# Kernel tuning notes

Hardware: AMD Instinct MI355X
Metric: run time of the kernel (lower is better)

Reference implementation:

```python
import jax, jax.numpy as jnp
import numpy as np

B, E, F, H, C = 2048, 16, 512, 1024, 512
TOP_K = 4
TEMP = 1.0


def setup_inputs() -> dict:
    key = jax.random.key(0)
    ks = jax.random.split(key, 5)
    h = jax.random.normal(ks[0], (B, F), jnp.float32)
    # Router posterior params (xavier-ish mu, logvar init at -7 as in torch code)
    W_mu = jax.random.normal(ks[1], (E, F), jnp.float32) * (1.0 / np.sqrt(F))
    W_logvar = jnp.full((E, F), -7.0, jnp.float32)
    b_mu = jnp.zeros((E,), jnp.float32)
    b_logvar = jnp.full((E,), -7.0, jnp.float32)
    # Expert MLP params: layer1 [F->H] relu, layer2 [H->C]
    W1 = jax.random.normal(ks[2], (E, F, H), jnp.float32) * (1.0 / np.sqrt(F))
    b1 = jnp.zeros((E, H), jnp.float32)
    W2 = jax.random.normal(ks[3], (E, H, C), jnp.float32) * (1.0 / np.sqrt(H))
    b2 = jnp.zeros((E, C), jnp.float32)
    return {"h": h, "W_mu": W_mu, "b_mu": b_mu, "W_logvar": W_logvar,
            "b_logvar": b_logvar, "W1": W1, "b1": b1, "W2": W2, "b2": b2}


def reference(h, W_mu, b_mu, W_logvar, b_logvar, W1, b1, W2, b2):
    # Bayesian router moments: mu = h @ W_mu^T + b_mu ; var = (h*h) @ exp(W_logvar)^T + exp(b_logvar)
    mu_m = h @ W_mu.T + b_mu                                   # [B,E]
    var_m = (h * h) @ jnp.exp(W_logvar).T + jnp.exp(b_logvar)  # [B,E]
    var_m = jnp.maximum(var_m, 1e-12)
    # Logistic-normal shrink: tilde = mu / sqrt(1 + (pi/8) var)
    tilde_m = mu_m / jnp.sqrt(1.0 + (jnp.pi / 8.0) * var_m)
    gate_probs = jax.nn.softmax(tilde_m / TEMP, axis=-1)       # [B,E]
    # Strict top-k by gate_scores (tilde_m), renormalize probs within top-k
    topk_scores, topk_idx = jax.lax.top_k(tilde_m, TOP_K)      # [B,k]
    topk_w = jnp.take_along_axis(gate_probs, topk_idx, axis=1) # [B,k]
    topk_w = topk_w / jnp.maximum(topk_w.sum(axis=1, keepdims=True), 1e-12)
    # Dense combine weights: w[b,e] = sum of renormalized top-k weights of token b for expert e
    Bsz = h.shape[0]
    w = jnp.zeros((Bsz, E), h.dtype).at[jnp.arange(Bsz)[:, None], topk_idx].add(topk_w)
    # Expert MLPs (grouped GEMM form); tokens not routed to expert e get weight 0
    a = jax.nn.relu(jnp.einsum('bf,efh->beh', h, W1) + b1)     # [B,E,H]
    y = jnp.einsum('beh,ehc->bec', a, W2) + b2                 # [B,E,C]
    combined = jnp.einsum('be,bec->bc', w, y)                  # [B,C]
    return combined
```

## Files before the change

kernel.cpp:

```cpp
#include <hip/hip_runtime.h>
#include <hip/hip_bf16.h>

typedef __attribute__((ext_vector_type(8))) short bf16x8;
typedef __attribute__((ext_vector_type(4))) float f32x4;

#define NTOK   2048
#define NEXP   16
#define NF     512
#define NH     1024
#define NCOUT  512
#define NPAIR  8192

__device__ __forceinline__ void gload16_lds(const __hip_bfloat16* g, const __hip_bfloat16* l) {
  __builtin_amdgcn_global_load_lds((const __attribute__((address_space(1))) void*)g,
                                   (__attribute__((address_space(3))) void*)l, 16, 0, 0);
}

__global__ __launch_bounds__(256) void precompute_kernel(
    const float* __restrict__ W_logvar, const float* __restrict__ b_logvar,
    float* __restrict__ expW, float* __restrict__ expb)
{
  int i = blockIdx.x * 256 + threadIdx.x;
  if (i < NEXP * NF) expW[i] = expf(W_logvar[i]);
  if (i < NEXP) expb[i] = expf(b_logvar[i]);
}

__global__ __launch_bounds__(256) void router_kernel(
    const float* __restrict__ h, const float* __restrict__ W_mu,
    const float* __restrict__ b_mu, const float* __restrict__ expW,
    const float* __restrict__ expb,
    int* __restrict__ topk_idx, float* __restrict__ topk_w,
    __hip_bfloat16* __restrict__ hb)
{
  __shared__ __align__(16) float hs[NF], hs2[NF];
  __shared__ float smu[NEXP], svar[NEXP];
  const int b = blockIdx.x, tid = threadIdx.x;
  for (int i = tid; i < NF; i += 256) {
    float v = h[(size_t)b * NF + i];
    hs[i] = v; hs2[i] = v * v;
    hb[(size_t)b * NF + i] = __float2bfloat16(v);
  }
  __syncthreads();
  const int e = tid >> 4, l = tid & 15;
  float mu = 0.f, var = 0.f;
  const float4* wm4 = (const float4*)(W_mu + e * NF);
  const float4* wv4 = (const float4*)(expW + e * NF);
  const float4* h4  = (const float4*)hs;
  const float4* h24 = (const float4*)hs2;
#pragma unroll
  for (int j = 0; j < NF / 64; ++j) {
    int i4 = l + j * 16;
    float4 a = h4[i4],  wa = wm4[i4];
    float4 c = h24[i4], wc = wv4[i4];
    mu  += a.x * wa.x + a.y * wa.y + a.z * wa.z + a.w * wa.w;
    var += c.x * wc.x + c.y * wc.y + c.z * wc.z + c.w * wc.w;
  }
#pragma unroll
  for (int o = 1; o < 16; o <<= 1) { mu += __shfl_xor(mu, o); var += __shfl_xor(var, o); }
  if (l == 0) { smu[e] = mu + b_mu[e]; svar[e] = var + expb[e]; }
  __syncthreads();
  if (tid < 64) {
    float val = -1e30f;
    if (tid < NEXP) {
      float v = fmaxf(svar[tid], 1e-12f);
      val = smu[tid] / sqrtf(1.0f + 0.39269908169872414f * v);
    }
    float mx = 0.f, wsum = 0.f;
    int i0, i1, i2, i3; float p0, p1, p2, p3;
#define TOPK_ROUND(ii, pp, FIRST)                                          \
    {                                                                      \
      float m = val;                                                       \
      m = fmaxf(m, __shfl_xor(m, 1));  m = fmaxf(m, __shfl_xor(m, 2));     \
      m = fmaxf(m, __shfl_xor(m, 4));  m = fmaxf(m, __shfl_xor(m, 8));     \
      m = fmaxf(m, __shfl_xor(m, 16)); m = fmaxf(m, __shfl_xor(m, 32));    \
      unsigned long long bm = __ballot(val == m);                          \
      int bi = (int)__builtin_ctzll(bm);                                   \
      if (FIRST) mx = m;                                                   \
      pp = expf(m - mx); wsum += pp; ii = bi;                              \
      if (tid == bi) val = -1e30f;                                         \
    }
    TOPK_ROUND(i0, p0, 1)
    TOPK_ROUND(i1, p1, 0)
    TOPK_ROUND(i2, p2, 0)
    TOPK_ROUND(i3, p3, 0)
#undef TOPK_ROUND
    if (tid == 0) {
      float inv = 1.0f / fmaxf(wsum, 1e-12f);
      topk_idx[b * 4 + 0] = i0; topk_w[b * 4 + 0] = p0 * inv;
      topk_idx[b * 4 + 1] = i1; topk_w[b * 4 + 1] = p1 * inv;
      topk_idx[b * 4 + 2] = i2; topk_w[b * 4 + 2] = p2 * inv;
      topk_idx[b * 4 + 3] = i3; topk_w[b * 4 + 3] = p3 * inv;
    }
  }
}

__global__ __launch_bounds__(1024) void route_finish_kernel(
    const int* __restrict__ topk_idx,
    int* __restrict__ counts, int* __restrict__ offsets,
    int* __restrict__ token_of_row, int* __restrict__ pair_row)
{
  __shared__ int cnt[128][16];
  __shared__ int choff[128][16];
  __shared__ int tot[16];
  __shared__ int soff[16];
  const int tid = threadIdx.x;
  const int wv = tid >> 6, ln = tid & 63;
  int mye[8], myrank[8];
#pragma unroll
  for (int r = 0; r < 8; ++r) {
    const int chunk = r * 16 + wv;
    const int t = chunk * 64 + ln;
    const int e = topk_idx[t];
    mye[r] = e;
    unsigned long long mymask = 0;
#pragma unroll
    for (int ee = 0; ee < 16; ++ee) {
      unsigned long long b = __ballot(e == ee);
      if (ln == 0) cnt[chunk][ee] = __popcll(b);
      if (e == ee) mymask = b;
    }
    myrank[r] = __popcll(mymask & ((1ull << ln) - 1ull));
  }
  __syncthreads();
  if (tid < 16) {
    int run = 0;
    for (int c = 0; c < 128; ++c) { choff[c][tid] = run; run += cnt[c][tid]; }
    tot[tid] = run;
    counts[tid] = run;
  }
  __syncthreads();
  if (tid == 0) {
    int run = 0;
    for (int e2 = 0; e2 < NEXP; ++e2) { soff[e2] = run; offsets[e2] = run; run += tot[e2]; }
  }
  __syncthreads();
#pragma unroll
  for (int r = 0; r < 8; ++r) {
    const int chunk = r * 16 + wv;
    const int t = chunk * 64 + ln;
    const int e = mye[r];
    const int pos = soff[e] + choff[chunk][e] + myrank[r];
    token_of_row[pos] = t >> 2;
    pair_row[t] = pos;
  }
}

__global__ __launch_bounds__(256) void transpose_convert_kernel(
    const float* __restrict__ in, __hip_bfloat16* __restrict__ out, int R, int C)
{
  __shared__ float tile[64][33];
  const int e = blockIdx.z;
  const int r0 = blockIdx.y * 64, c0 = blockIdx.x * 32;
  const int x = threadIdx.x & 31, y = threadIdx.x >> 5;
  const float* ip = in + ((size_t)e * R + r0) * C + c0;
#pragma unroll
  for (int i = 0; i < 8; ++i) tile[y + 8 * i][x] = ip[(size_t)(y + 8 * i) * C + x];
  __syncthreads();
  const int rp = threadIdx.x & 31, cb = threadIdx.x >> 5;
#pragma unroll
  for (int j = 0; j < 4; ++j) {
    const int c = cb + 8 * j;
    union { __hip_bfloat16 b[2]; unsigned u; } v;
    v.b[0] = __float2bfloat16(tile[2 * rp][c]);
    v.b[1] = __float2bfloat16(tile[2 * rp + 1][c]);
    *(unsigned*)(out + ((size_t)e * C + c0 + c) * R + r0 + 2 * rp) = v.u;
  }
}


__global__ __launch_bounds__(256) void gemm1_kernel(
    const __hip_bfloat16* __restrict__ hb,
    const __hip_bfloat16* __restrict__ W1t,
    const float* __restrict__ b1,
    const int* __restrict__ token_of_row, const int* __restrict__ offsets,
    const int* __restrict__ counts,
    __hip_bfloat16* __restrict__ a_out)
{
  const int bid = blockIdx.x;
  const int id  = (bid & 7) * 512 + (bid >> 3);
  const int e   = id >> 8;
  const int m0  = ((id >> 4) & 15) * 128;
  const int n0  = (id & 15) * 64;
  const int cnt = counts[e];
  if (m0 >= cnt) return;
  const int off = offsets[e];

  __shared__ __align__(16) __hip_bfloat16 As[2][128 * 64];
  __shared__ __align__(16) __hip_bfloat16 Bs[2][64 * 64];

  const int tid = threadIdx.x;
  const int w = tid >> 6, l = tid & 63;
  const int wm = w >> 1, wn = w & 1;
  const int r16 = l & 15, g4 = l >> 4;
  const int sx = r16 & 7;
  const int koffL = (((l & 7) ^ (l >> 3)) * 8);

  const __hip_bfloat16* Aptr[4];
#pragma unroll
  for (int i = 0; i < 4; ++i) {
    int r = off + m0 + w * 32 + i * 8 + (l >> 3);
    if (r > NPAIR - 1) r = NPAIR - 1;
    Aptr[i] = hb + (size_t)token_of_row[r] * NF + koffL;
  }
  const __hip_bfloat16* Bptr[2];
#pragma unroll
  for (int i = 0; i < 2; ++i)
    Bptr[i] = W1t + ((size_t)e * NH + n0 + w * 16 + i * 8 + (l >> 3)) * NF + koffL;

#define STG1(b, k0) { \
  _Pragma("unroll") for (int i = 0; i < 4; ++i) gload16_lds(Aptr[i] + (k0), &As[b][(w * 32 + i * 8) * 64]); \
  _Pragma("unroll") for (int i = 0; i < 2; ++i) gload16_lds(Bptr[i] + (k0), &Bs[b][(w * 16 + i * 8) * 64]); }

  f32x4 acc[4][2] = {};
  const int NT = NF / 64;

  STG1(0, 0)
  for (int t = 0; t < NT; ++t) {
    __syncthreads();
    const int cur = t & 1;
    if (t + 1 < NT) STG1(cur ^ 1, (t + 1) * 64)
#pragma unroll
    for (int ks = 0; ks < 2; ++ks) {
      const int seg = (ks * 4 + g4) ^ sx;
      bf16x8 af[4], bq[2];
#pragma unroll
      for (int rr = 0; rr < 4; ++rr)
        af[rr] = *(const bf16x8*)(&As[cur][(wm * 64 + rr * 16 + r16) * 64 + seg * 8]);
#pragma unroll
      for (int nn = 0; nn < 2; ++nn)
        bq[nn] = *(const bf16x8*)(&Bs[cur][(wn * 32 + nn * 16 + r16) * 64 + seg * 8]);
#pragma unroll
      for (int rr = 0; rr < 4; ++rr)
#pragma unroll
        for (int nn = 0; nn < 2; ++nn)
          acc[rr][nn] = __builtin_amdgcn_mfma_f32_16x16x32_bf16(af[rr], bq[nn], acc[rr][nn], 0, 0, 0);
    }
  }
#undef STG1

  const int q4 = l >> 4, cl = l & 15;
  const int mmax = cnt - m0;
#pragma unroll
  for (int rr = 0; rr < 4; ++rr) {
#pragma unroll
    for (int nn = 0; nn < 2; ++nn) {
      const int c = n0 + wn * 32 + nn * 16 + cl;
      const float bias = b1[e * NH + c];
#pragma unroll
      for (int q = 0; q < 4; ++q) {
        const int r = wm * 64 + rr * 16 + q4 * 4 + q;
        if (r < mmax) {
          float v = fmaxf(acc[rr][nn][q] + bias, 0.f);
          a_out[(size_t)(off + m0 + r) * NH + c] = __float2bfloat16(v);
        }
      }
    }
  }
}

__global__ __launch_bounds__(256) void gemm2_kernel(
    const __hip_bfloat16* __restrict__ a_in,
    const __hip_bfloat16* __restrict__ W2t,
    const float* __restrict__ b2,
    const int* __restrict__ offsets, const int* __restrict__ counts,
    float* __restrict__ ybuf)
{
  const int bid = blockIdx.x;
  const int id  = (bid & 7) * 256 + (bid >> 3);
  const int e   = id >> 7;
  const int m0  = ((id >> 3) & 15) * 128;
  const int n0  = (id & 7) * 64;
  const int cnt = counts[e];
  if (m0 >= cnt) return;
  const int off = offsets[e];

  __shared__ __align__(16) __hip_bfloat16 As[2][128 * 64];
  __shared__ __align__(16) __hip_bfloat16 Bs[2][64 * 64];

  const int tid = threadIdx.x;
  const int w = tid >> 6, l = tid & 63;
  const int wm = w >> 1, wn = w & 1;
  const int r16 = l & 15, g4 = l >> 4;
  const int sx = r16 & 7;
  const int koffL = (((l & 7) ^ (l >> 3)) * 8);

  const __hip_bfloat16* Aptr[4];
#pragma unroll
  for (int i = 0; i < 4; ++i) {
    int r = off + m0 + w * 32 + i * 8 + (l >> 3);
    if (r > NPAIR - 1) r = NPAIR - 1;
    Aptr[i] = a_in + (size_t)r * NH + koffL;
  }
  const __hip_bfloat16* Bptr[2];
#pragma unroll
  for (int i = 0; i < 2; ++i)
    Bptr[i] = W2t + ((size_t)e * NCOUT + n0 + w * 16 + i * 8 + (l >> 3)) * NH + koffL;

#define STG2(b, k0) { \
  _Pragma("unroll") for (int i = 0; i < 4; ++i) gload16_lds(Aptr[i] + (k0), &As[b][(w * 32 + i * 8) * 64]); \
  _Pragma("unroll") for (int i = 0; i < 2; ++i) gload16_lds(Bptr[i] + (k0), &Bs[b][(w * 16 + i * 8) * 64]); }

  f32x4 acc[4][2] = {};
  const int NT = NH / 64;

  STG2(0, 0)
  for (int t = 0; t < NT; ++t) {
    __syncthreads();
    const int cur = t & 1;
    if (t + 1 < NT) STG2(cur ^ 1, (t + 1) * 64)
#pragma unroll
    for (int ks = 0; ks < 2; ++ks) {
      const int seg = (ks * 4 + g4) ^ sx;
      bf16x8 af[4], bq[2];
#pragma unroll
      for (int rr = 0; rr < 4; ++rr)
        af[rr] = *(const bf16x8*)(&As[cur][(wm * 64 + rr * 16 + r16) * 64 + seg * 8]);
#pragma unroll
      for (int nn = 0; nn < 2; ++nn)
        bq[nn] = *(const bf16x8*)(&Bs[cur][(wn * 32 + nn * 16 + r16) * 64 + seg * 8]);
#pragma unroll
      for (int rr = 0; rr < 4; ++rr)
#pragma unroll
        for (int nn = 0; nn < 2; ++nn)
          acc[rr][nn] = __builtin_amdgcn_mfma_f32_16x16x32_bf16(af[rr], bq[nn], acc[rr][nn], 0, 0, 0);
    }
  }
#undef STG2

  const int q4 = l >> 4, cl = l & 15;
  const int mmax = cnt - m0;
#pragma unroll
  for (int rr = 0; rr < 4; ++rr) {
#pragma unroll
    for (int nn = 0; nn < 2; ++nn) {
      const int c = n0 + wn * 32 + nn * 16 + cl;
      const float bias = b2[e * NCOUT + c];
#pragma unroll
      for (int q = 0; q < 4; ++q) {
        const int r = wm * 64 + rr * 16 + q4 * 4 + q;
        if (r < mmax)
          ybuf[(size_t)(off + m0 + r) * NCOUT + c] = acc[rr][nn][q] + bias;
      }
    }
  }
}

__global__ __launch_bounds__(256) void combine_kernel(
    const float* __restrict__ ybuf, const int* __restrict__ pair_row,
    const float* __restrict__ topk_w, float* __restrict__ out)
{
  const int tok = blockIdx.x;
  const int c = threadIdx.x * 2;
  float a0 = 0.f, a1 = 0.f;
#pragma unroll
  for (int k = 0; k < 4; ++k) {
    const int t = tok * 4 + k;
    const float wt = topk_w[t];
    const float2 y = *(const float2*)(ybuf + (size_t)pair_row[t] * NCOUT + c);
    a0 += wt * y.x; a1 += wt * y.y;
  }
  *(float2*)(out + (size_t)tok * NCOUT + c) = make_float2(a0, a1);
}

extern "C" void kernel_launch(void* const* d_in, const int* in_sizes, int n_in,
                              void* d_out, int out_size, void* d_ws, size_t ws_size,
                              hipStream_t stream) {
  (void)in_sizes; (void)n_in; (void)ws_size; (void)out_size;
  const float* h        = (const float*)d_in[0];
  const float* W_mu     = (const float*)d_in[1];
  const float* b_mu     = (const float*)d_in[2];
  const float* W_logvar = (const float*)d_in[3];
  const float* b_logvar = (const float*)d_in[4];
  const float* W1       = (const float*)d_in[5];
  const float* b1       = (const float*)d_in[6];
  const float* W2       = (const float*)d_in[7];
  const float* b2       = (const float*)d_in[8];
  float* out = (float*)d_out;

  char* p = (char*)d_ws;
  int*   counts   = (int*)p;   p += 16 * 4;
  int*   offsets  = (int*)p;   p += 16 * 4;
  float* expb     = (float*)p; p += 16 * 4;
  p += 16 * 4;
  float* expW     = (float*)p; p += (size_t)NEXP * NF * 4;
  int*   topk_idx = (int*)p;   p += (size_t)NPAIR * 4;
  float* topk_w   = (float*)p; p += (size_t)NPAIR * 4;
  int*   tok_row  = (int*)p;   p += (size_t)NPAIR * 4;
  int*   pair_row = (int*)p;   p += (size_t)NPAIR * 4;
  __hip_bfloat16* hb   = (__hip_bfloat16*)p; p += (size_t)NTOK * NF * 2;
  __hip_bfloat16* W1t  = (__hip_bfloat16*)p; p += (size_t)NEXP * NF * NH * 2;
  __hip_bfloat16* W2t  = (__hip_bfloat16*)p; p += (size_t)NEXP * NH * NCOUT * 2;
  __hip_bfloat16* abuf = (__hip_bfloat16*)p; p += (size_t)NPAIR * NH * 2;
  float*          ybuf = (float*)p;          p += (size_t)NPAIR * NCOUT * 4;

  precompute_kernel<<<(NEXP * NF + 255) / 256, 256, 0, stream>>>(W_logvar, b_logvar, expW, expb);
  router_kernel<<<NTOK, 256, 0, stream>>>(h, W_mu, b_mu, expW, expb, topk_idx, topk_w, hb);
  route_finish_kernel<<<1, 1024, 0, stream>>>(topk_idx, counts, offsets, tok_row, pair_row);

  transpose_convert_kernel<<<dim3(NH / 32, NF / 64, NEXP), 256, 0, stream>>>(W1, W1t, NF, NH);
  transpose_convert_kernel<<<dim3(NCOUT / 32, NH / 64, NEXP), 256, 0, stream>>>(W2, W2t, NH, NCOUT);

  gemm1_kernel<<<4096, 256, 0, stream>>>(hb, W1t, b1, tok_row, offsets, counts, abuf);
  gemm2_kernel<<<2048, 256, 0, stream>>>(abuf, W2t, b2, offsets, counts, ybuf);
  combine_kernel<<<NTOK, 256, 0, stream>>>(ybuf, pair_row, topk_w, out);
}
```

Baseline: 102.6 us.

## Fuse exp into router, split route_finish across blocks, single-buffer GEMM staging

Drops the separate precompute kernel and computes exp of the logvar weights inside the router, removing one launch at the cost of redundant exp work per token block. route_finish now runs on 8 blocks, each scattering rows for two experts while recomputing the shared counts. Both GEMM kernels switch from double-buffered LDS staging to a single buffer with a sync on each side of the load. This cuts LDS use and may raise occupancy, but load latency is no longer hidden behind MFMA work.

```diff
diff --git a/kernel.cpp b/kernel.cpp
--- a/kernel.cpp
+++ b/kernel.cpp
@@ -16,19 +16,10 @@
                                    (__attribute__((address_space(3))) void*)l, 16, 0, 0);
 }
 
-__global__ __launch_bounds__(256) void precompute_kernel(
-    const float* __restrict__ W_logvar, const float* __restrict__ b_logvar,
-    float* __restrict__ expW, float* __restrict__ expb)
-{
-  int i = blockIdx.x * 256 + threadIdx.x;
-  if (i < NEXP * NF) expW[i] = expf(W_logvar[i]);
-  if (i < NEXP) expb[i] = expf(b_logvar[i]);
-}
-
 __global__ __launch_bounds__(256) void router_kernel(
     const float* __restrict__ h, const float* __restrict__ W_mu,
-    const float* __restrict__ b_mu, const float* __restrict__ expW,
-    const float* __restrict__ expb,
+    const float* __restrict__ b_mu, const float* __restrict__ W_logvar,
+    const float* __restrict__ b_logvar,
     int* __restrict__ topk_idx, float* __restrict__ topk_w,
     __hip_bfloat16* __restrict__ hb)
 {
@@ -44,7 +35,7 @@
   const int e = tid >> 4, l = tid & 15;
   float mu = 0.f, var = 0.f;
   const float4* wm4 = (const float4*)(W_mu + e * NF);
-  const float4* wv4 = (const float4*)(expW + e * NF);
+  const float4* wv4 = (const float4*)(W_logvar + e * NF);
   const float4* h4  = (const float4*)hs;
   const float4* h24 = (const float4*)hs2;
 #pragma unroll
@@ -53,11 +44,11 @@
     float4 a = h4[i4],  wa = wm4[i4];
     float4 c = h24[i4], wc = wv4[i4];
     mu  += a.x * wa.x + a.y * wa.y + a.z * wa.z + a.w * wa.w;
-    var += c.x * wc.x + c.y * wc.y + c.z * wc.z + c.w * wc.w;
+    var += c.x * __expf(wc.x) + c.y * __expf(wc.y) + c.z * __expf(wc.z) + c.w * __expf(wc.w);
   }
 #pragma unroll
   for (int o = 1; o < 16; o <<= 1) { mu += __shfl_xor(mu, o); var += __shfl_xor(var, o); }
-  if (l == 0) { smu[e] = mu + b_mu[e]; svar[e] = var + expb[e]; }
+  if (l == 0) { smu[e] = mu + b_mu[e]; svar[e] = var + __expf(b_logvar[e]); }
   __syncthreads();
   if (tid < 64) {
     float val = -1e30f;
@@ -100,11 +91,12 @@
     int* __restrict__ token_of_row, int* __restrict__ pair_row)
 {
   __shared__ int cnt[128][16];
-  __shared__ int choff[128][16];
+  __shared__ int choff[128][2];
   __shared__ int tot[16];
   __shared__ int soff[16];
   const int tid = threadIdx.x;
   const int wv = tid >> 6, ln = tid & 63;
+  const int e0 = blockIdx.x * 2;
   int mye[8], myrank[8];
 #pragma unroll
   for (int r = 0; r < 8; ++r) {
@@ -115,33 +107,44 @@
     unsigned long long mymask = 0;
 #pragma unroll
     for (int ee = 0; ee < 16; ++ee) {
-      unsigned long long b = __ballot(e == ee);
-      if (ln == 0) cnt[chunk][ee] = __popcll(b);
-      if (e == ee) mymask = b;
+      unsigned long long bmask = __ballot(e == ee);
+      if (ln == 0) cnt[chunk][ee] = __popcll(bmask);
+      if (e == ee) mymask = bmask;
     }
     myrank[r] = __popcll(mymask & ((1ull << ln) - 1ull));
   }
   __syncthreads();
   if (tid < 16) {
     int run = 0;
-    for (int c = 0; c < 128; ++c) { choff[c][tid] = run; run += cnt[c][tid]; }
+    for (int c = 0; c < 128; ++c) run += cnt[c][tid];
     tot[tid] = run;
-    counts[tid] = run;
+    if (blockIdx.x == 0) counts[tid] = run;
+  }
+  if (tid >= 32 && tid < 34) {
+    const int e = e0 + (tid - 32);
+    int run = 0;
+    for (int c = 0; c < 128; ++c) { choff[c][tid - 32] = run; run += cnt[c][e]; }
   }
   __syncthreads();
   if (tid == 0) {
     int run = 0;
-    for (int e2 = 0; e2 < NEXP; ++e2) { soff[e2] = run; offsets[e2] = run; run += tot[e2]; }
+    for (int e2 = 0; e2 < NEXP; ++e2) {
+      soff[e2] = run;
+      if (blockIdx.x == 0) offsets[e2] = run;
+      run += tot[e2];
+    }
   }
   __syncthreads();
 #pragma unroll
   for (int r = 0; r < 8; ++r) {
-    const int chunk = r * 16 + wv;
-    const int t = chunk * 64 + ln;
     const int e = mye[r];
-    const int pos = soff[e] + choff[chunk][e] + myrank[r];
-    token_of_row[pos] = t >> 2;
-    pair_row[t] = pos;
+    if (e == e0 || e == e0 + 1) {
+      const int chunk = r * 16 + wv;
+      const int t = chunk * 64 + ln;
+      const int pos = soff[e] + choff[chunk][e - e0] + myrank[r];
+      token_of_row[pos] = t >> 2;
+      pair_row[t] = pos;
+    }
   }
 }
 
@@ -185,8 +188,8 @@
   if (m0 >= cnt) return;
   const int off = offsets[e];
 
-  __shared__ __align__(16) __hip_bfloat16 As[2][128 * 64];
-  __shared__ __align__(16) __hip_bfloat16 Bs[2][64 * 64];
+  __shared__ __align__(16) __hip_bfloat16 As[128 * 64];
+  __shared__ __align__(16) __hip_bfloat16 Bs[64 * 64];
 
   const int tid = threadIdx.x;
   const int w = tid >> 6, l = tid & 63;
@@ -207,28 +210,25 @@
   for (int i = 0; i < 2; ++i)
     Bptr[i] = W1t + ((size_t)e * NH + n0 + w * 16 + i * 8 + (l >> 3)) * NF + koffL;
 
-#define STG1(b, k0) { \
-  _Pragma("unroll") for (int i = 0; i < 4; ++i) gload16_lds(Aptr[i] + (k0), &As[b][(w * 32 + i * 8) * 64]); \
-  _Pragma("unroll") for (int i = 0; i < 2; ++i) gload16_lds(Bptr[i] + (k0), &Bs[b][(w * 16 + i * 8) * 64]); }
-
   f32x4 acc[4][2] = {};
-  const int NT = NF / 64;
-
-  STG1(0, 0)
-  for (int t = 0; t < NT; ++t) {
+
+  for (int k0 = 0; k0 < NF; k0 += 64) {
     __syncthreads();
-    const int cur = t & 1;
-    if (t + 1 < NT) STG1(cur ^ 1, (t + 1) * 64)
+#pragma unroll
+    for (int i = 0; i < 4; ++i) gload16_lds(Aptr[i] + k0, As + (w * 32 + i * 8) * 64);
+#pragma unroll
+    for (int i = 0; i < 2; ++i) gload16_lds(Bptr[i] + k0, Bs + (w * 16 + i * 8) * 64);
+    __syncthreads();
 #pragma unroll
     for (int ks = 0; ks < 2; ++ks) {
       const int seg = (ks * 4 + g4) ^ sx;
       bf16x8 af[4], bq[2];
 #pragma unroll
       for (int rr = 0; rr < 4; ++rr)
-        af[rr] = *(const bf16x8*)(&As[cur][(wm * 64 + rr * 16 + r16) * 64 + seg * 8]);
+        af[rr] = *(const bf16x8*)(As + (wm * 64 + rr * 16 + r16) * 64 + seg * 8);
 #pragma unroll
       for (int nn = 0; nn < 2; ++nn)
-        bq[nn] = *(const bf16x8*)(&Bs[cur][(wn * 32 + nn * 16 + r16) * 64 + seg * 8]);
+        bq[nn] = *(const bf16x8*)(Bs + (wn * 32 + nn * 16 + r16) * 64 + seg * 8);
 #pragma unroll
       for (int rr = 0; rr < 4; ++rr)
 #pragma unroll
@@ -236,7 +236,6 @@
           acc[rr][nn] = __builtin_amdgcn_mfma_f32_16x16x32_bf16(af[rr], bq[nn], acc[rr][nn], 0, 0, 0);
     }
   }
-#undef STG1
 
   const int q4 = l >> 4, cl = l & 15;
   const int mmax = cnt - m0;
@@ -274,8 +273,8 @@
   if (m0 >= cnt) return;
   const int off = offsets[e];
 
-  __shared__ __align__(16) __hip_bfloat16 As[2][128 * 64];
-  __shared__ __align__(16) __hip_bfloat16 Bs[2][64 * 64];
+  __shared__ __align__(16) __hip_bfloat16 As[128 * 64];
+  __shared__ __align__(16) __hip_bfloat16 Bs[64 * 64];
 
   const int tid = threadIdx.x;
   const int w = tid >> 6, l = tid & 63;
@@ -296,28 +295,25 @@
   for (int i = 0; i < 2; ++i)
     Bptr[i] = W2t + ((size_t)e * NCOUT + n0 + w * 16 + i * 8 + (l >> 3)) * NH + koffL;
 
-#define STG2(b, k0) { \
-  _Pragma("unroll") for (int i = 0; i < 4; ++i) gload16_lds(Aptr[i] + (k0), &As[b][(w * 32 + i * 8) * 64]); \
-  _Pragma("unroll") for (int i = 0; i < 2; ++i) gload16_lds(Bptr[i] + (k0), &Bs[b][(w * 16 + i * 8) * 64]); }
-
   f32x4 acc[4][2] = {};
-  const int NT = NH / 64;
-
-  STG2(0, 0)
-  for (int t = 0; t < NT; ++t) {
+
+  for (int k0 = 0; k0 < NH; k0 += 64) {
     __syncthreads();
-    const int cur = t & 1;
-    if (t + 1 < NT) STG2(cur ^ 1, (t + 1) * 64)
+#pragma unroll
+    for (int i = 0; i < 4; ++i) gload16_lds(Aptr[i] + k0, As + (w * 32 + i * 8) * 64);
+#pragma unroll
+    for (int i = 0; i < 2; ++i) gload16_lds(Bptr[i] + k0, Bs + (w * 16 + i * 8) * 64);
+    __syncthreads();
 #pragma unroll
     for (int ks = 0; ks < 2; ++ks) {
       const int seg = (ks * 4 + g4) ^ sx;
       bf16x8 af[4], bq[2];
 #pragma unroll
       for (int rr = 0; rr < 4; ++rr)
-        af[rr] = *(const bf16x8*)(&As[cur][(wm * 64 + rr * 16 + r16) * 64 + seg * 8]);
+        af[rr] = *(const bf16x8*)(As + (wm * 64 + rr * 16 + r16) * 64 + seg * 8);
 #pragma unroll
       for (int nn = 0; nn < 2; ++nn)
-        bq[nn] = *(const bf16x8*)(&Bs[cur][(wn * 32 + nn * 16 + r16) * 64 + seg * 8]);
+        bq[nn] = *(const bf16x8*)(Bs + (wn * 32 + nn * 16 + r16) * 64 + seg * 8);
 #pragma unroll
       for (int rr = 0; rr < 4; ++rr)
 #pragma unroll
@@ -325,7 +321,6 @@
           acc[rr][nn] = __builtin_amdgcn_mfma_f32_16x16x32_bf16(af[rr], bq[nn], acc[rr][nn], 0, 0, 0);
     }
   }
-#undef STG2
 
   const int q4 = l >> 4, cl = l & 15;
   const int mmax = cnt - m0;
@@ -380,9 +375,7 @@
   char* p = (char*)d_ws;
   int*   counts   = (int*)p;   p += 16 * 4;
   int*   offsets  = (int*)p;   p += 16 * 4;
-  float* expb     = (float*)p; p += 16 * 4;
-  p += 16 * 4;
-  float* expW     = (float*)p; p += (size_t)NEXP * NF * 4;
+  p += 32 * 4;
   int*   topk_idx = (int*)p;   p += (size_t)NPAIR * 4;
   float* topk_w   = (float*)p; p += (size_t)NPAIR * 4;
   int*   tok_row  = (int*)p;   p += (size_t)NPAIR * 4;
@@ -393,9 +386,9 @@
   __hip_bfloat16* abuf = (__hip_bfloat16*)p; p += (size_t)NPAIR * NH * 2;
   float*          ybuf = (float*)p;          p += (size_t)NPAIR * NCOUT * 4;
 
-  precompute_kernel<<<(NEXP * NF + 255) / 256, 256, 0, stream>>>(W_logvar, b_logvar, expW, expb);
-  router_kernel<<<NTOK, 256, 0, stream>>>(h, W_mu, b_mu, expW, expb, topk_idx, topk_w, hb);
-  route_finish_kernel<<<1, 1024, 0, stream>>>(topk_idx, counts, offsets, tok_row, pair_row);
+  router_kernel<<<NTOK, 256, 0, stream>>>(h, W_mu, b_mu, W_logvar, b_logvar,
+                                          topk_idx, topk_w, hb);
+  route_finish_kernel<<<8, 1024, 0, stream>>>(topk_idx, counts, offsets, tok_row, pair_row);
 
   transpose_convert_kernel<<<dim3(NH / 32, NF / 64, NEXP), 256, 0, stream>>>(W1, W1t, NF, NH);
   transpose_convert_kernel<<<dim3(NCOUT / 32, NH / 64, NEXP), 256, 0, stream>>>(W2, W2t, NH, NCOUT);
```

After: 92.87 us. -9.5%, faster.
